# Kernel tuning notes

Hardware: AMD Instinct MI355X
Metric: run time of the kernel (lower is better)

## Reference

```python
import jax, jax.numpy as jnp
import numpy as np

TWO_PI = 2.0 * np.pi


def setup_inputs() -> dict:
    key = jax.random.key(0)
    k_h, k_y, k_yw, k_yb, k_uw, k_ub = jax.random.split(key, 6)
    B, F, Cin, Cout, D = 4, 128, 64, 8, 3
    NX = NY = NZ = 48
    omega = 30.0
    h = jax.random.normal(k_h, (B, F, Cin), dtype=jnp.float32)
    y = jax.random.uniform(k_y, (B, NX, NY, NZ, D), dtype=jnp.float32)
    # y_linear: weight initialized ~ U(-1/sqrt(D), 1/sqrt(D)) then scaled by omega
    y_w = jax.random.uniform(k_yw, (F, D), dtype=jnp.float32, minval=-1.0, maxval=1.0) / np.sqrt(D) * omega
    y_b = jax.random.uniform(k_yb, (F,), dtype=jnp.float32, minval=-1.0, maxval=1.0) / np.sqrt(D)
    u_w = jax.random.uniform(k_uw, (Cout, Cin), dtype=jnp.float32, minval=-1.0, maxval=1.0) / np.sqrt(Cin)
    u_b = jax.random.uniform(k_ub, (Cout,), dtype=jnp.float32, minval=-1.0, maxval=1.0) / np.sqrt(Cin)
    return {"h": h, "y": y, "y_w": y_w, "y_b": y_b, "u_w": u_w, "u_b": u_b}


def reference(h, y, y_w, y_b, u_w, u_b):
    # Y = y_linear(y): (b, x, y, z, f)
    Y = jnp.einsum('bxyzd,fd->bxyzf', y, y_w) + y_b
    # Real part of exp(2j*pi*Y) contracted with real h == contraction with cos(2*pi*Y)
    C = jnp.cos(TWO_PI * Y)                                  # (b,x,y,z,f)
    U = jnp.einsum('bfm,bxyzf->bxyzm', h, C)                  # (b,x,y,z,Cin)
    n_grid = y.shape[1] * y.shape[2] * y.shape[3]
    U = jnp.sin(U / n_grid)                                   # activ_fn = sin
    return jnp.einsum('bxyzm,om->bxyzo', U, u_w) + u_b        # (b,x,y,z,Cout)
```

## Files before the change

### kernel.cpp

```cpp
#include <hip/hip_runtime.h>
#include <hip/hip_bf16.h>


#define NPTS      110592
#define NFREQ     128
#define CIN       64
#define COUT      8
#define PTS_BLK   256
#define BLK_PER_B (NPTS / PTS_BLK)
#define GT_STRIDE 136

typedef __bf16 bf16x8 __attribute__((ext_vector_type(8)));
typedef float  f32x4  __attribute__((ext_vector_type(4)));

__global__ __launch_bounds__(256) void spectral_prep(
    const float* __restrict__ h,
    const float* __restrict__ u_w,
    const float* __restrict__ y_w,
    const float* __restrict__ y_b,
    __bf16* __restrict__ gws,
    float4* __restrict__ pkws)
{
    int b  = blockIdx.x >> 3;
    int fg = blockIdx.x & 7;
    int t  = threadIdx.x;
    int f  = fg * 16 + (t >> 4);
    int n  = t & 15;

    float acc = 0.0f;
    if (n < COUT) {
        const float4* hp = (const float4*)(h + ((size_t)(b * NFREQ + f)) * CIN);
        const float4* up = (const float4*)(u_w + (size_t)n * CIN);
#pragma unroll
        for (int m = 0; m < CIN / 4; ++m) {
            float4 a = hp[m], c = up[m];
            acc += a.x * c.x + a.y * c.y + a.z * c.z + a.w * c.w;
        }
        acc *= (1.0f / (float)NPTS);
    }
    gws[(size_t)b * (16 * NFREQ) + n * NFREQ + f] = (__bf16)acc;

    if (blockIdx.x == 0 && t < NFREQ) {
        pkws[t] = make_float4(y_w[3 * t], y_w[3 * t + 1], y_w[3 * t + 2], y_b[t]);
    }
}

__global__ __launch_bounds__(256, 4) void spectral_main(
    const float*  __restrict__ y,
    const __bf16* __restrict__ gws,
    const float4* __restrict__ pkws,
    const float*  __restrict__ u_b,
    float*        __restrict__ out)
{
    __shared__ __align__(16) __bf16 GT_lds[16 * GT_STRIDE];
    __shared__ __align__(16) float4 pk_lds[NFREQ];
    __shared__ __align__(16) float  y_lds[PTS_BLK * 3];

    const int t     = threadIdx.x;
    const int b     = blockIdx.x / BLK_PER_B;
    const int pbase = (blockIdx.x % BLK_PER_B) * PTS_BLK;

    {
        bf16x8 g = ((const bf16x8*)(gws + (size_t)b * (16 * NFREQ)))[t];
        *(bf16x8*)&GT_lds[(t >> 4) * GT_STRIDE + (t & 15) * 8] = g;
        if (t < NFREQ) pk_lds[t] = pkws[t];
        if (t < PTS_BLK * 3 / 4)
            ((float4*)y_lds)[t] = ((const float4*)(y + ((size_t)b * NPTS + pbase) * 3))[t];
    }
    __syncthreads();

    const int lane = t & 63;
    const int wv   = t >> 6;
    const int quad = lane >> 4;
    const int l15  = lane & 15;

    float yc[4][3];
#pragma unroll
    for (int rt = 0; rt < 4; ++rt) {
        int p = wv * 64 + rt * 16 + l15;
        yc[rt][0] = y_lds[p * 3 + 0];
        yc[rt][1] = y_lds[p * 3 + 1];
        yc[rt][2] = y_lds[p * 3 + 2];
    }

    f32x4 acc[4] = {{0,0,0,0},{0,0,0,0},{0,0,0,0},{0,0,0,0}};
    const __bf16* bptr = &GT_lds[l15 * GT_STRIDE + quad * 8];
    const float4* wp   = &pk_lds[quad * 8];

#pragma unroll
    for (int k0 = 0; k0 < NFREQ; k0 += 32) {
        bf16x8 a0, a1, a2, a3;
#pragma unroll
        for (int j = 0; j < 8; ++j) {
            float4 w = wp[k0 + j];
            float Y0 = __builtin_fmaf(w.x, yc[0][0], __builtin_fmaf(w.y, yc[0][1], __builtin_fmaf(w.z, yc[0][2], w.w)));
            float Y1 = __builtin_fmaf(w.x, yc[1][0], __builtin_fmaf(w.y, yc[1][1], __builtin_fmaf(w.z, yc[1][2], w.w)));
            float Y2 = __builtin_fmaf(w.x, yc[2][0], __builtin_fmaf(w.y, yc[2][1], __builtin_fmaf(w.z, yc[2][2], w.w)));
            float Y3 = __builtin_fmaf(w.x, yc[3][0], __builtin_fmaf(w.y, yc[3][1], __builtin_fmaf(w.z, yc[3][2], w.w)));
            a0[j] = (__bf16)__builtin_amdgcn_cosf(__builtin_amdgcn_fractf(Y0));
            a1[j] = (__bf16)__builtin_amdgcn_cosf(__builtin_amdgcn_fractf(Y1));
            a2[j] = (__bf16)__builtin_amdgcn_cosf(__builtin_amdgcn_fractf(Y2));
            a3[j] = (__bf16)__builtin_amdgcn_cosf(__builtin_amdgcn_fractf(Y3));
        }
        bf16x8 bf = *(const bf16x8*)(bptr + k0);
        acc[0] = __builtin_amdgcn_mfma_f32_16x16x32_bf16(a0, bf, acc[0], 0, 0, 0);
        acc[1] = __builtin_amdgcn_mfma_f32_16x16x32_bf16(a1, bf, acc[1], 0, 0, 0);
        acc[2] = __builtin_amdgcn_mfma_f32_16x16x32_bf16(a2, bf, acc[2], 0, 0, 0);
        acc[3] = __builtin_amdgcn_mfma_f32_16x16x32_bf16(a3, bf, acc[3], 0, 0, 0);
    }

    if (l15 < COUT) {
        float ub = u_b[l15];
        size_t base = ((size_t)b * NPTS + pbase) * COUT;
#pragma unroll
        for (int rt = 0; rt < 4; ++rt) {
#pragma unroll
            for (int q = 0; q < 4; ++q) {
                int pr = wv * 64 + rt * 16 + quad * 4 + q;
                out[base + (size_t)pr * COUT + l15] = acc[rt][q] + ub;
            }
        }
    }
}

extern "C" void kernel_launch(void* const* d_in, const int* in_sizes, int n_in,
                              void* d_out, int out_size, void* d_ws, size_t ws_size,
                              hipStream_t stream)
{
    const float* h   = (const float*)d_in[0];
    const float* y   = (const float*)d_in[1];
    const float* y_w = (const float*)d_in[2];
    const float* y_b = (const float*)d_in[3];
    const float* u_w = (const float*)d_in[4];
    const float* u_b = (const float*)d_in[5];
    float* out = (float*)d_out;
    __bf16* gws  = (__bf16*)d_ws;
    float4* pkws = (float4*)((char*)d_ws + 16384);

    spectral_prep<<<32, 256, 0, stream>>>(h, u_w, y_w, y_b, gws, pkws);
    spectral_main<<<4 * BLK_PER_B, 256, 0, stream>>>(y, gws, pkws, u_b, out);
}
```

Baseline: 85.38 us.

## Replace MFMA bf16 path with scalar fp32 packed-FMA per-point loop

Drops the bf16 MFMA contraction and shared-memory staging. Each thread now handles two points directly, computing cos per frequency and accumulating 8 outputs with packed fp32 FMAs against a per-batch table that interleaves frequency weights, bias and folded h·u_w coefficients. Reading the table through uniform global loads and writing outputs as float4 removes LDS traffic and syncs. The cost is that the reduction over frequencies now runs on the vector ALUs instead of the matrix cores, which adds more FMA work per point.

```diff
diff --git a/kernel.cpp b/kernel.cpp
--- a/kernel.cpp
+++ b/kernel.cpp
@@ -1,126 +1,109 @@
 #include <hip/hip_runtime.h>
-#include <hip/hip_bf16.h>
 
 
 #define NPTS      110592
 #define NFREQ     128
 #define CIN       64
 #define COUT      8
-#define PTS_BLK   256
+#define THR       128
+#define P_PER_T   2
+#define PTS_BLK   (THR * P_PER_T)
 #define BLK_PER_B (NPTS / PTS_BLK)
-#define GT_STRIDE 136
 
-typedef __bf16 bf16x8 __attribute__((ext_vector_type(8)));
-typedef float  f32x4  __attribute__((ext_vector_type(4)));
+typedef float f32x2 __attribute__((ext_vector_type(2)));
 
 __global__ __launch_bounds__(256) void spectral_prep(
     const float* __restrict__ h,
     const float* __restrict__ u_w,
     const float* __restrict__ y_w,
     const float* __restrict__ y_b,
-    __bf16* __restrict__ gws,
-    float4* __restrict__ pkws)
+    float* __restrict__ T)
 {
-    int b  = blockIdx.x >> 3;
-    int fg = blockIdx.x & 7;
-    int t  = threadIdx.x;
-    int f  = fg * 16 + (t >> 4);
-    int n  = t & 15;
+    __shared__ float uw[COUT * CIN];
+    const int t = threadIdx.x;
+    for (int i = t; i < COUT * CIN; i += 256) uw[i] = u_w[i];
+    __syncthreads();
 
-    float acc = 0.0f;
-    if (n < COUT) {
-        const float4* hp = (const float4*)(h + ((size_t)(b * NFREQ + f)) * CIN);
-        const float4* up = (const float4*)(u_w + (size_t)n * CIN);
+    const int id = blockIdx.x * 256 + t;
+    const int b = id >> 7, f = id & 127;
+
+    const float4* hp = (const float4*)(h + ((size_t)(b * NFREQ + f)) * CIN);
+    float g[COUT] = {0, 0, 0, 0, 0, 0, 0, 0};
+    for (int m4 = 0; m4 < CIN / 4; ++m4) {
+        float4 a = hp[m4];
 #pragma unroll
-        for (int m = 0; m < CIN / 4; ++m) {
-            float4 a = hp[m], c = up[m];
-            acc += a.x * c.x + a.y * c.y + a.z * c.z + a.w * c.w;
+        for (int o = 0; o < COUT; ++o) {
+            float4 u = *(const float4*)&uw[o * CIN + m4 * 4];
+            g[o] += a.x * u.x + a.y * u.y + a.z * u.z + a.w * u.w;
         }
-        acc *= (1.0f / (float)NPTS);
     }
-    gws[(size_t)b * (16 * NFREQ) + n * NFREQ + f] = (__bf16)acc;
-
-    if (blockIdx.x == 0 && t < NFREQ) {
-        pkws[t] = make_float4(y_w[3 * t], y_w[3 * t + 1], y_w[3 * t + 2], y_b[t]);
-    }
+    float* dst = T + (size_t)id * 12;
+    dst[0] = y_w[f * 3 + 0];
+    dst[1] = y_w[f * 3 + 1];
+    dst[2] = y_w[f * 3 + 2];
+    dst[3] = y_b[f];
+#pragma unroll
+    for (int o = 0; o < COUT; ++o) dst[4 + o] = g[o] * (1.0f / (float)NPTS);
 }
 
-__global__ __launch_bounds__(256, 4) void spectral_main(
-    const float*  __restrict__ y,
-    const __bf16* __restrict__ gws,
-    const float4* __restrict__ pkws,
-    const float*  __restrict__ u_b,
-    float*        __restrict__ out)
+__global__ __launch_bounds__(THR) void spectral_main(
+    const float* __restrict__ y,
+    const float* __restrict__ T,
+    const float* __restrict__ u_b,
+    float*       __restrict__ out)
 {
-    __shared__ __align__(16) __bf16 GT_lds[16 * GT_STRIDE];
-    __shared__ __align__(16) float4 pk_lds[NFREQ];
-    __shared__ __align__(16) float  y_lds[PTS_BLK * 3];
-
     const int t     = threadIdx.x;
     const int b     = blockIdx.x / BLK_PER_B;
     const int pbase = (blockIdx.x % BLK_PER_B) * PTS_BLK;
+    const int p0    = pbase + t;
+    const int p1    = pbase + THR + t;
 
-    {
-        bf16x8 g = ((const bf16x8*)(gws + (size_t)b * (16 * NFREQ)))[t];
-        *(bf16x8*)&GT_lds[(t >> 4) * GT_STRIDE + (t & 15) * 8] = g;
-        if (t < NFREQ) pk_lds[t] = pkws[t];
-        if (t < PTS_BLK * 3 / 4)
-            ((float4*)y_lds)[t] = ((const float4*)(y + ((size_t)b * NPTS + pbase) * 3))[t];
-    }
-    __syncthreads();
+    const float* yp = y + (size_t)b * NPTS * 3;
+    f32x2 X  = {yp[p0 * 3 + 0], yp[p1 * 3 + 0]};
+    f32x2 Yc = {yp[p0 * 3 + 1], yp[p1 * 3 + 1]};
+    f32x2 Z  = {yp[p0 * 3 + 2], yp[p1 * 3 + 2]};
 
-    const int lane = t & 63;
-    const int wv   = t >> 6;
-    const int quad = lane >> 4;
-    const int l15  = lane & 15;
+    const float* Tb = T + (size_t)b * NFREQ * 12;
 
-    float yc[4][3];
+    f32x2 accA[4] = {{0, 0}, {0, 0}, {0, 0}, {0, 0}};
+    f32x2 accB[4] = {{0, 0}, {0, 0}, {0, 0}, {0, 0}};
+
+#pragma unroll 4
+    for (int f = 0; f < NFREQ; ++f) {
+        const float* tf = Tb + f * 12;
+        float wx = tf[0], wy = tf[1], wz = tf[2], wb = tf[3];
+        f32x2 Yv = __builtin_elementwise_fma((f32x2){wx, wx}, X,
+                   __builtin_elementwise_fma((f32x2){wy, wy}, Yc,
+                   __builtin_elementwise_fma((f32x2){wz, wz}, Z,
+                                             (f32x2){wb, wb})));
+        float c0 = __builtin_amdgcn_cosf(__builtin_amdgcn_fractf(Yv[0]));
+        float c1 = __builtin_amdgcn_cosf(__builtin_amdgcn_fractf(Yv[1]));
+        f32x2 cc0 = {c0, c0}, cc1 = {c1, c1};
 #pragma unroll
-    for (int rt = 0; rt < 4; ++rt) {
-        int p = wv * 64 + rt * 16 + l15;
-        yc[rt][0] = y_lds[p * 3 + 0];
-        yc[rt][1] = y_lds[p * 3 + 1];
-        yc[rt][2] = y_lds[p * 3 + 2];
+        for (int oo = 0; oo < 4; ++oo) {
+            f32x2 g = *(const f32x2*)(tf + 4 + 2 * oo);
+            accA[oo] = __builtin_elementwise_fma(cc0, g, accA[oo]);
+            accB[oo] = __builtin_elementwise_fma(cc1, g, accB[oo]);
+        }
     }
 
-    f32x4 acc[4] = {{0,0,0,0},{0,0,0,0},{0,0,0,0},{0,0,0,0}};
-    const __bf16* bptr = &GT_lds[l15 * GT_STRIDE + quad * 8];
-    const float4* wp   = &pk_lds[quad * 8];
+    float ub[COUT];
+#pragma unroll
+    for (int o = 0; o < COUT; ++o) ub[o] = u_b[o];
 
-#pragma unroll
-    for (int k0 = 0; k0 < NFREQ; k0 += 32) {
-        bf16x8 a0, a1, a2, a3;
-#pragma unroll
-        for (int j = 0; j < 8; ++j) {
-            float4 w = wp[k0 + j];
-            float Y0 = __builtin_fmaf(w.x, yc[0][0], __builtin_fmaf(w.y, yc[0][1], __builtin_fmaf(w.z, yc[0][2], w.w)));
-            float Y1 = __builtin_fmaf(w.x, yc[1][0], __builtin_fmaf(w.y, yc[1][1], __builtin_fmaf(w.z, yc[1][2], w.w)));
-            float Y2 = __builtin_fmaf(w.x, yc[2][0], __builtin_fmaf(w.y, yc[2][1], __builtin_fmaf(w.z, yc[2][2], w.w)));
-            float Y3 = __builtin_fmaf(w.x, yc[3][0], __builtin_fmaf(w.y, yc[3][1], __builtin_fmaf(w.z, yc[3][2], w.w)));
-            a0[j] = (__bf16)__builtin_amdgcn_cosf(__builtin_amdgcn_fractf(Y0));
-            a1[j] = (__bf16)__builtin_amdgcn_cosf(__builtin_amdgcn_fractf(Y1));
-            a2[j] = (__bf16)__builtin_amdgcn_cosf(__builtin_amdgcn_fractf(Y2));
-            a3[j] = (__bf16)__builtin_amdgcn_cosf(__builtin_amdgcn_fractf(Y3));
-        }
-        bf16x8 bf = *(const bf16x8*)(bptr + k0);
-        acc[0] = __builtin_amdgcn_mfma_f32_16x16x32_bf16(a0, bf, acc[0], 0, 0, 0);
-        acc[1] = __builtin_amdgcn_mfma_f32_16x16x32_bf16(a1, bf, acc[1], 0, 0, 0);
-        acc[2] = __builtin_amdgcn_mfma_f32_16x16x32_bf16(a2, bf, acc[2], 0, 0, 0);
-        acc[3] = __builtin_amdgcn_mfma_f32_16x16x32_bf16(a3, bf, acc[3], 0, 0, 0);
-    }
-
-    if (l15 < COUT) {
-        float ub = u_b[l15];
-        size_t base = ((size_t)b * NPTS + pbase) * COUT;
-#pragma unroll
-        for (int rt = 0; rt < 4; ++rt) {
-#pragma unroll
-            for (int q = 0; q < 4; ++q) {
-                int pr = wv * 64 + rt * 16 + quad * 4 + q;
-                out[base + (size_t)pr * COUT + l15] = acc[rt][q] + ub;
-            }
-        }
-    }
+    const size_t obase = (size_t)b * NPTS * COUT;
+    float4 vA0 = {accA[0][0] + ub[0], accA[0][1] + ub[1],
+                  accA[1][0] + ub[2], accA[1][1] + ub[3]};
+    float4 vA1 = {accA[2][0] + ub[4], accA[2][1] + ub[5],
+                  accA[3][0] + ub[6], accA[3][1] + ub[7]};
+    float4 vB0 = {accB[0][0] + ub[0], accB[0][1] + ub[1],
+                  accB[1][0] + ub[2], accB[1][1] + ub[3]};
+    float4 vB1 = {accB[2][0] + ub[4], accB[2][1] + ub[5],
+                  accB[3][0] + ub[6], accB[3][1] + ub[7]};
+    *(float4*)(out + obase + (size_t)p0 * COUT)     = vA0;
+    *(float4*)(out + obase + (size_t)p0 * COUT + 4) = vA1;
+    *(float4*)(out + obase + (size_t)p1 * COUT)     = vB0;
+    *(float4*)(out + obase + (size_t)p1 * COUT + 4) = vB1;
 }
 
 extern "C" void kernel_launch(void* const* d_in, const int* in_sizes, int n_in,
@@ -134,9 +117,8 @@
     const float* u_w = (const float*)d_in[4];
     const float* u_b = (const float*)d_in[5];
     float* out = (float*)d_out;
-    __bf16* gws  = (__bf16*)d_ws;
-    float4* pkws = (float4*)((char*)d_ws + 16384);
+    float* T   = (float*)d_ws;
 
-    spectral_prep<<<32, 256, 0, stream>>>(h, u_w, y_w, y_b, gws, pkws);
-    spectral_main<<<4 * BLK_PER_B, 256, 0, stream>>>(y, gws, pkws, u_b, out);
+    spectral_prep<<<2, 256, 0, stream>>>(h, u_w, y_w, y_b, T);
+    spectral_main<<<4 * BLK_PER_B, THR, 0, stream>>>(y, T, u_b, out);
 }
```

Measured after the change: 93.55 us. +9.6%, slower.
